# Optimization experiments

Measured on AMD Instinct MI355X. Metric: run time of the kernel, lower is better.

The kernel has to match this reference:

```python
import jax, jax.numpy as jnp
import numpy as np

V, D, H, DH, FF, L = 512, 256, 8, 32, 2048, 2
B, S = 4, 128
EPS = 1e-5


def setup_inputs() -> dict:
    key = jax.random.key(0)
    ks = jax.random.split(key, 8)
    rn = lambda k, shape: jax.random.normal(k, shape, jnp.float32) * 0.02
    return {
        "x_t": jax.random.randint(ks[0], (B, S), 0, V),
        "emb": rn(ks[1], (V, D)),
        "temperature": jnp.array(1.0, jnp.float32),
        "Wq": rn(ks[2], (L, D, D)), "Wk": rn(ks[3], (L, D, D)),
        "Wv": rn(ks[4], (L, D, D)), "Wo": rn(ks[5], (L, D, D)),
        "bq": jnp.zeros((L, D)), "bk": jnp.zeros((L, D)),
        "bv": jnp.zeros((L, D)), "bo": jnp.zeros((L, D)),
        "W1": rn(ks[6], (L, D, FF)), "b1": jnp.zeros((L, FF)),
        "W2": rn(ks[7], (L, FF, D)), "b2": jnp.zeros((L, D)),
        "ln1_s": jnp.ones((L, D)), "ln1_b": jnp.zeros((L, D)),
        "ln2_s": jnp.ones((L, D)), "ln2_b": jnp.zeros((L, D)),
    }


def _layer_norm(x, scale, bias):
    m = jnp.mean(x, axis=-1, keepdims=True)
    v = jnp.var(x, axis=-1, keepdims=True)
    return (x - m) / jnp.sqrt(v + EPS) * scale + bias


def reference(x_t, emb, temperature, Wq, Wk, Wv, Wo, bq, bk, bv, bo,
              W1, b1, W2, b2, ln1_s, ln1_b, ln2_s, ln2_b):
    b, s = x_t.shape
    x = emb[x_t]  # [B,S,D]
    scale = 1.0 / np.sqrt(DH).astype(np.float32)
    for l in range(L):  # 2 structurally distinct layers (post-norm, ReLU FFN)
        q = (x @ Wq[l] + bq[l]).reshape(b, s, H, DH)
        k = (x @ Wk[l] + bk[l]).reshape(b, s, H, DH)
        v = (x @ Wv[l] + bv[l]).reshape(b, s, H, DH)
        scores = jnp.einsum('bqhd,bkhd->bhqk', q, k) * scale
        attn = jax.nn.softmax(scores, axis=-1)
        o = jnp.einsum('bhqk,bkhd->bqhd', attn, v).reshape(b, s, D)
        x = _layer_norm(x + (o @ Wo[l] + bo[l]), ln1_s[l], ln1_b[l])
        ff = jax.nn.relu(x @ W1[l] + b1[l]) @ W2[l] + b2[l]
        x = _layer_norm(x + ff, ln2_s[l], ln2_b[l])
    sim = (x @ emb.T) / temperature            # [B,S,V]
    tp = jax.nn.softmax(sim, axis=-1)          # [B,S,V]
    # torch loop `trans_matrix[:,:,i,:] = transition_probs` == broadcast over row dim
    return jnp.broadcast_to(tp[:, :, None, :], (b, s, V, V))
```

## Files before the change

### kernel.cpp

```cpp
#include <hip/hip_runtime.h>
#include <math.h>

#define V_  512
#define D_  256
#define H_  8
#define DH_ 32
#define FF_ 2048
#define L_  2
#define B_  4
#define S_  128
#define T_  (B_*S_)

typedef float f32x4 __attribute__((ext_vector_type(4)));
typedef short s16x8 __attribute__((ext_vector_type(8)));
typedef unsigned short u16x4 __attribute__((ext_vector_type(4)));
typedef unsigned short ushort_t;

__device__ __forceinline__ ushort_t f2b(float f) {
    unsigned int u = __builtin_bit_cast(unsigned int, f);
    u += 0x7FFFu + ((u >> 16) & 1u);
    return (ushort_t)(u >> 16);
}
__device__ __forceinline__ float b2f(ushort_t h) {
    unsigned int u = ((unsigned int)h) << 16;
    return __builtin_bit_cast(float, u);
}

__device__ __forceinline__ float waveReduceSum(float v) {
#pragma unroll
    for (int off = 32; off > 0; off >>= 1) v += __shfl_xor(v, off);
    return v;
}
__device__ __forceinline__ float waveReduceMax(float v) {
#pragma unroll
    for (int off = 32; off > 0; off >>= 1) v = fmaxf(v, __shfl_xor(v, off));
    return v;
}

template<int RELU, int OUTB, int BIAS>
__device__ __forceinline__ void mgemm_body(
    const ushort_t* __restrict__ A, const ushort_t* __restrict__ BT,
    const float* __restrict__ bias, float* __restrict__ Cf,
    ushort_t* __restrict__ Cb, int M, int N, int K, int kBegin, int kSteps)
{
    __shared__ ushort_t Al[64][40];
    __shared__ ushort_t Bl[64][40];
    const int tid  = threadIdx.x;
    const int m0   = blockIdx.y * 64, n0 = blockIdx.x * 64;
    const int lane = tid & 63, w = tid >> 6;
    const int srow = tid >> 2, sseg = (tid & 3) * 8;
    const int l15  = lane & 15,  kg = (lane >> 4) * 8;

    f32x4 acc0 = {0.f,0.f,0.f,0.f}, acc1 = acc0, acc2 = acc0, acc3 = acc0;

    for (int kt = 0; kt < kSteps; ++kt) {
        const int k0 = kBegin + kt * 32;
        s16x8 av = *(const s16x8*)&A [(size_t)(m0 + srow) * K + k0 + sseg];
        s16x8 bv = *(const s16x8*)&BT[(size_t)(n0 + srow) * K + k0 + sseg];
        __syncthreads();
        *(s16x8*)&Al[srow][sseg] = av;
        *(s16x8*)&Bl[srow][sseg] = bv;
        __syncthreads();
        s16x8 bfr = *(const s16x8*)&Bl[w * 16 + l15][kg];
        s16x8 a0  = *(const s16x8*)&Al[     l15][kg];
        s16x8 a1  = *(const s16x8*)&Al[16 + l15][kg];
        s16x8 a2  = *(const s16x8*)&Al[32 + l15][kg];
        s16x8 a3  = *(const s16x8*)&Al[48 + l15][kg];
        acc0 = __builtin_amdgcn_mfma_f32_16x16x32_bf16(a0, bfr, acc0, 0, 0, 0);
        acc1 = __builtin_amdgcn_mfma_f32_16x16x32_bf16(a1, bfr, acc1, 0, 0, 0);
        acc2 = __builtin_amdgcn_mfma_f32_16x16x32_bf16(a2, bfr, acc2, 0, 0, 0);
        acc3 = __builtin_amdgcn_mfma_f32_16x16x32_bf16(a3, bfr, acc3, 0, 0, 0);
    }

    const int col = n0 + w * 16 + l15;
    const float bb = BIAS ? bias[col] : 0.f;
    f32x4 accs[4] = {acc0, acc1, acc2, acc3};
#pragma unroll
    for (int r = 0; r < 4; ++r) {
#pragma unroll
        for (int e = 0; e < 4; ++e) {
            const int row = m0 + r * 16 + (lane >> 4) * 4 + e;
            float v = accs[r][e] + bb;
            if (RELU) v = fmaxf(v, 0.f);
            if (OUTB) Cb[(size_t)row * N + col] = f2b(v);
            else      Cf[(size_t)row * N + col] = v;
        }
    }
}

template<int RELU, int OUTB, int BIAS>
__global__ __launch_bounds__(256) void mgemm_k(const ushort_t* A, const ushort_t* BT,
    const float* bias, float* Cf0, float* Cf1, ushort_t* Cb,
    int M, int N, int K, int kChunk)
{
    const int z = blockIdx.z;
    float* Cfz = nullptr;
    if (Cf0) Cfz = (z < 2) ? Cf0 + (size_t)z * M * N
                           : Cf1 + (size_t)(z - 2) * M * N;
    mgemm_body<RELU, OUTB, BIAS>(A, BT, bias, Cfz, Cb, M, N, K,
                                 z * kChunk, kChunk / 32);
}

__global__ __launch_bounds__(256) void qkv_k(const ushort_t* Xb, const ushort_t* WT,
    const float* bq, const float* bk, const float* bv,
    ushort_t* Qb, ushort_t* Kb, ushort_t* Vb)
{
    const int z = blockIdx.z;
    const ushort_t* bt = WT + (size_t)z * (D_ * D_);
    const float* bias; ushort_t* out;
    if (z == 0)      { bias = bq; out = Qb; }
    else if (z == 1) { bias = bk; out = Kb; }
    else             { bias = bv; out = Vb; }
    mgemm_body<0, 1, 1>(Xb, bt, bias, nullptr, out, T_, D_, D_, 0, D_ / 32);
}

__global__ __launch_bounds__(256) void prep_k(const int* __restrict__ xt,
    const float* __restrict__ emb, float* __restrict__ X,
    ushort_t* __restrict__ Xb, ushort_t* __restrict__ embB,
    const float* __restrict__ Wq, const float* __restrict__ Wk,
    const float* __restrict__ Wv, const float* __restrict__ Wo,
    const float* __restrict__ W1, const float* __restrict__ W2,
    ushort_t* __restrict__ WT, ushort_t* __restrict__ W1T, ushort_t* __restrict__ W2T)
{
    __shared__ float Tl[32][33];
    const int tid = threadIdx.x;
    if (blockIdx.x < 512) {
        const int idx = blockIdx.x * 256 + tid;
        const int t = idx >> 8, d = idx & 255;
        const float v = emb[(size_t)xt[t] * D_ + d];
        X[idx]  = v;
        Xb[idx] = f2b(v);
        embB[idx] = f2b(emb[idx]);
        return;
    }
    const int id = blockIdx.x - 512;
    const int l  = id >= 1280 ? 1 : 0;
    const int t  = id - l * 1280;
    const float* src; ushort_t* dst; int R, C, rt, ct;
    if (t < 256) {
        const int kind = t >> 6, tl = t & 63;
        const float* s0 = (kind == 0) ? Wq : (kind == 1) ? Wk : (kind == 2) ? Wv : Wo;
        src = s0 + (size_t)l * (D_ * D_);
        dst = WT + (size_t)l * (4 * D_ * D_) + (size_t)kind * (D_ * D_);
        R = D_; C = D_; rt = tl >> 3; ct = tl & 7;
    } else if (t < 768) {
        const int tl = t - 256;
        src = W1 + (size_t)l * (D_ * FF_); dst = W1T + (size_t)l * (D_ * FF_);
        R = D_; C = FF_; rt = tl >> 6; ct = tl & 63;
    } else {
        const int tl = t - 768;
        src = W2 + (size_t)l * (FF_ * D_); dst = W2T + (size_t)l * (FF_ * D_);
        R = FF_; C = D_; rt = tl >> 3; ct = tl & 7;
    }
    const int r = tid >> 3, c4 = (tid & 7) * 4;
    f32x4 v = *(const f32x4*)&src[(size_t)(rt * 32 + r) * C + ct * 32 + c4];
    Tl[r][c4] = v[0]; Tl[r][c4 + 1] = v[1]; Tl[r][c4 + 2] = v[2]; Tl[r][c4 + 3] = v[3];
    __syncthreads();
    u16x4 ov;
    ov[0] = f2b(Tl[c4 + 0][r]); ov[1] = f2b(Tl[c4 + 1][r]);
    ov[2] = f2b(Tl[c4 + 2][r]); ov[3] = f2b(Tl[c4 + 3][r]);
    *(u16x4*)&dst[(size_t)(ct * 32 + r) * R + rt * 32 + c4] = ov;
}

__global__ __launch_bounds__(256) void add_ln_k(
    const float* __restrict__ p0, const float* __restrict__ p1, int nparts,
    const float* __restrict__ bias, float* __restrict__ X,
    ushort_t* __restrict__ Xb, const float* __restrict__ s,
    const float* __restrict__ b)
{
    __shared__ float red[4];
    const int row = blockIdx.x, tid = threadIdx.x;
    const size_t off = (size_t)row * D_ + tid;
    const size_t TD = (size_t)T_ * D_;
    float a = X[off] + bias[tid] + p0[off];
    if (nparts == 4) a += p0[TD + off] + p1[off] + p1[TD + off];

    float ws_ = waveReduceSum(a);
    if ((tid & 63) == 0) red[tid >> 6] = ws_;
    __syncthreads();
    const float mean = (red[0] + red[1] + red[2] + red[3]) * (1.f / D_);
    __syncthreads();
    const float d = a - mean;
    float vs = waveReduceSum(d * d);
    if ((tid & 63) == 0) red[tid >> 6] = vs;
    __syncthreads();
    const float var = (red[0] + red[1] + red[2] + red[3]) * (1.f / D_);
    const float y = d * rsqrtf(var + 1e-5f) * s[tid] + b[tid];
    X[off]  = y;
    Xb[off] = f2b(y);
}

__global__ __launch_bounds__(256) void attn_k(const ushort_t* __restrict__ Qb,
    const ushort_t* __restrict__ Kb, const ushort_t* __restrict__ Vb,
    ushort_t* __restrict__ Ob)
{
    __shared__ float Qs[32][36], Ks[128][36], Vs[128][36], Ps[32][132];
    const int bh = blockIdx.x, b = bh >> 3, h = bh & 7;
    const int i0 = blockIdx.y * 32;
    const int tid = threadIdx.x;

#pragma unroll
    for (int it = 0; it < 2; ++it) {
        const int g = it * 256 + tid;
        const int r = g >> 2, c8 = (g & 3) * 8;
        s16x8 kv = *(const s16x8*)&Kb[(size_t)(b * S_ + r) * D_ + h * DH_ + c8];
        s16x8 vv = *(const s16x8*)&Vb[(size_t)(b * S_ + r) * D_ + h * DH_ + c8];
        f32x4 klo = {b2f((ushort_t)kv[0]), b2f((ushort_t)kv[1]), b2f((ushort_t)kv[2]), b2f((ushort_t)kv[3])};
        f32x4 khi = {b2f((ushort_t)kv[4]), b2f((ushort_t)kv[5]), b2f((ushort_t)kv[6]), b2f((ushort_t)kv[7])};
        f32x4 vlo = {b2f((ushort_t)vv[0]), b2f((ushort_t)vv[1]), b2f((ushort_t)vv[2]), b2f((ushort_t)vv[3])};
        f32x4 vhi = {b2f((ushort_t)vv[4]), b2f((ushort_t)vv[5]), b2f((ushort_t)vv[6]), b2f((ushort_t)vv[7])};
        *(f32x4*)&Ks[r][c8]     = klo;  *(f32x4*)&Ks[r][c8 + 4] = khi;
        *(f32x4*)&Vs[r][c8]     = vlo;  *(f32x4*)&Vs[r][c8 + 4] = vhi;
    }
    if (tid < 128) {
        const int r = tid >> 2, c8 = (tid & 3) * 8;
        s16x8 qv = *(const s16x8*)&Qb[(size_t)(b * S_ + i0 + r) * D_ + h * DH_ + c8];
        f32x4 qlo = {b2f((ushort_t)qv[0]), b2f((ushort_t)qv[1]), b2f((ushort_t)qv[2]), b2f((ushort_t)qv[3])};
        f32x4 qhi = {b2f((ushort_t)qv[4]), b2f((ushort_t)qv[5]), b2f((ushort_t)qv[6]), b2f((ushort_t)qv[7])};
        *(f32x4*)&Qs[r][c8] = qlo;  *(f32x4*)&Qs[r][c8 + 4] = qhi;
    }
    __syncthreads();

    const int i = tid >> 3, jg = tid & 7;
    const float sc = 0.17677669529663687f;
    float sv[16];
    float mx = -1e30f;
#pragma unroll
    for (int jj = 0; jj < 16; ++jj) {
        const int j = jg + jj * 8;
        f32x4 a4 = {0.f,0.f,0.f,0.f};
#pragma unroll
        for (int kk = 0; kk < 8; ++kk) {
            f32x4 q = *(const f32x4*)&Qs[i][kk * 4];
            f32x4 k = *(const f32x4*)&Ks[j][kk * 4];
            a4 += q * k;
        }
        const float sdot = (a4[0] + a4[1] + a4[2] + a4[3]) * sc;
        sv[jj] = sdot;
        mx = fmaxf(mx, sdot);
    }
    mx = fmaxf(mx, __shfl_xor(mx, 1));
    mx = fmaxf(mx, __shfl_xor(mx, 2));
    mx = fmaxf(mx, __shfl_xor(mx, 4));
    float sum = 0.f;
#pragma unroll
    for (int jj = 0; jj < 16; ++jj) {
        const float e = __expf(sv[jj] - mx);
        Ps[i][jg + jj * 8] = e;
        sum += e;
    }
    sum += __shfl_xor(sum, 1);
    sum += __shfl_xor(sum, 2);
    sum += __shfl_xor(sum, 4);
    const float inv = 1.f / sum;
    __syncthreads();

    const int dg = tid & 7;
    f32x4 o = {0.f,0.f,0.f,0.f};
#pragma unroll 4
    for (int j = 0; j < 128; ++j) {
        const float p = Ps[i][j];
        f32x4 vv = *(const f32x4*)&Vs[j][dg * 4];
        o += vv * p;
    }
    u16x4 ov;
    ov[0] = f2b(o[0] * inv); ov[1] = f2b(o[1] * inv);
    ov[2] = f2b(o[2] * inv); ov[3] = f2b(o[3] * inv);
    *(u16x4*)&Ob[(size_t)(b * S_ + i0 + i) * D_ + h * DH_ + dg * 4] = ov;
}

__global__ __launch_bounds__(256) void bcast_k(const float* __restrict__ Lg,
    const float* __restrict__ temp, float* __restrict__ out)
{
    __shared__ float row[V_];
    __shared__ float red[4];
    const int blk = blockIdx.x, t = blk >> 2, quarter = blk & 3;
    const int tid = threadIdx.x;
    const float rT = 1.f / temp[0];
    const float l0 = Lg[(size_t)t * V_ + tid] * rT;
    const float l1 = Lg[(size_t)t * V_ + 256 + tid] * rT;
    float m = waveReduceMax(fmaxf(l0, l1));
    if ((tid & 63) == 0) red[tid >> 6] = m;
    __syncthreads();
    m = fmaxf(fmaxf(red[0], red[1]), fmaxf(red[2], red[3]));
    __syncthreads();
    const float e0 = __expf(l0 - m), e1 = __expf(l1 - m);
    float sblk = waveReduceSum(e0 + e1);
    if ((tid & 63) == 0) red[tid >> 6] = sblk;
    __syncthreads();
    const float inv = 1.f / (red[0] + red[1] + red[2] + red[3]);
    row[tid] = e0 * inv;
    row[tid + 256] = e1 * inv;
    __syncthreads();

    const int c = tid & 127, ihalf = tid >> 7;
    f32x4 v = *(const f32x4*)&row[c * 4];
    f32x4* dst = (f32x4*)out + (size_t)t * V_ * (V_ / 4);
#pragma unroll 4
    for (int r = 0; r < 64; ++r) {
        const int i = quarter * 128 + ihalf + r * 2;
        __builtin_nontemporal_store(v, &dst[(size_t)i * (V_ / 4) + c]);
    }
}

extern "C" void kernel_launch(void* const* d_in, const int* in_sizes, int n_in,
                              void* d_out, int out_size, void* d_ws, size_t ws_size,
                              hipStream_t stream)
{
    const int*   x_t  = (const int*)  d_in[0];
    const float* emb  = (const float*)d_in[1];
    const float* temp = (const float*)d_in[2];
    const float* Wq   = (const float*)d_in[3];
    const float* Wk   = (const float*)d_in[4];
    const float* Wv   = (const float*)d_in[5];
    const float* Wo   = (const float*)d_in[6];
    const float* bq   = (const float*)d_in[7];
    const float* bk   = (const float*)d_in[8];
    const float* bv   = (const float*)d_in[9];
    const float* bo   = (const float*)d_in[10];
    const float* W1   = (const float*)d_in[11];
    const float* b1   = (const float*)d_in[12];
    const float* W2   = (const float*)d_in[13];
    const float* b2   = (const float*)d_in[14];
    const float* ln1s = (const float*)d_in[15];
    const float* ln1b = (const float*)d_in[16];
    const float* ln2s = (const float*)d_in[17];
    const float* ln2b = (const float*)d_in[18];

    float* out = (float*)d_out;
    char*  wsb = (char*)d_ws;

    float*    X     = (float*)   (wsb + 0);
    float*    PartA = (float*)   (wsb + 524288);
    float*    Lg    = PartA;
    ushort_t* Qb    = (ushort_t*)(wsb + 1572864);
    float*    PartB = (float*)   (wsb + 1572864);
    ushort_t* Kb    = (ushort_t*)(wsb + 1835008);
    ushort_t* Vb    = (ushort_t*)(wsb + 2097152);
    ushort_t* Ob    = (ushort_t*)(wsb + 2359296);
    ushort_t* Xb    = (ushort_t*)(wsb + 2621440);
    ushort_t* Ffb   = (ushort_t*)(wsb + 2883584);
    ushort_t* embB  = (ushort_t*)(wsb + 4980736);
    ushort_t* WT    = (ushort_t*)(wsb + 5242880);
    ushort_t* W1T   = (ushort_t*)(wsb + 6291456);
    ushort_t* W2T   = (ushort_t*)(wsb + 8388608);

    prep_k<<<3072, 256, 0, stream>>>(x_t, emb, X, Xb, embB,
                                     Wq, Wk, Wv, Wo, W1, W2, WT, W1T, W2T);

    for (int l = 0; l < L_; ++l) {
        const ushort_t* WTl  = WT  + (size_t)l * (4 * D_ * D_);
        const ushort_t* W1Tl = W1T + (size_t)l * (D_ * FF_);
        const ushort_t* W2Tl = W2T + (size_t)l * (FF_ * D_);

        qkv_k<<<dim3(4, 8, 3), 256, 0, stream>>>(
            Xb, WTl, bq + l * D_, bk + l * D_, bv + l * D_, Qb, Kb, Vb);

        attn_k<<<dim3(32, 4), 256, 0, stream>>>(Qb, Kb, Vb, Ob);

        mgemm_k<0, 0, 0><<<dim3(4, 8, 1), 256, 0, stream>>>(
            Ob, WTl + 3 * D_ * D_, nullptr, PartA, nullptr, nullptr,
            T_, D_, D_, D_);
        add_ln_k<<<T_, 256, 0, stream>>>(PartA, nullptr, 1, bo + l * D_,
                                         X, Xb, ln1s + l * D_, ln1b + l * D_);

        mgemm_k<1, 1, 1><<<dim3(32, 8, 1), 256, 0, stream>>>(
            Xb, W1Tl, b1 + l * FF_, nullptr, nullptr, Ffb, T_, FF_, D_, D_);

        mgemm_k<0, 0, 0><<<dim3(4, 8, 4), 256, 0, stream>>>(
            Ffb, W2Tl, nullptr, PartA, PartB, nullptr, T_, D_, FF_, FF_ / 4);
        add_ln_k<<<T_, 256, 0, stream>>>(PartA, PartB, 4, b2 + l * D_,
                                         X, Xb, ln2s + l * D_, ln2b + l * D_);
    }

    mgemm_k<0, 0, 0><<<dim3(8, 8, 1), 256, 0, stream>>>(
        Xb, embB, nullptr, Lg, nullptr, nullptr, T_, V_, D_, D_);

    bcast_k<<<T_ * 4, 256, 0, stream>>>(Lg, temp, out);
}
```

Baseline: 187.9 us.

## Double-buffer LDS tiles in MFMA GEMM to overlap global loads with compute

```diff
diff --git a/kernel.cpp b/kernel.cpp
--- a/kernel.cpp
+++ b/kernel.cpp
@@ -43,8 +43,8 @@
     const float* __restrict__ bias, float* __restrict__ Cf,
     ushort_t* __restrict__ Cb, int M, int N, int K, int kBegin, int kSteps)
 {
-    __shared__ ushort_t Al[64][40];
-    __shared__ ushort_t Bl[64][40];
+    __shared__ ushort_t Al[2][64][40];
+    __shared__ ushort_t Bl[2][64][40];
     const int tid  = threadIdx.x;
     const int m0   = blockIdx.y * 64, n0 = blockIdx.x * 64;
     const int lane = tid & 63, w = tid >> 6;
@@ -53,23 +53,37 @@
 
     f32x4 acc0 = {0.f,0.f,0.f,0.f}, acc1 = acc0, acc2 = acc0, acc3 = acc0;
 
+    const ushort_t* Aptr = &A [(size_t)(m0 + srow) * K + kBegin + sseg];
+    const ushort_t* Bptr = &BT[(size_t)(n0 + srow) * K + kBegin + sseg];
+
+    s16x8 av = *(const s16x8*)Aptr;
+    s16x8 bv = *(const s16x8*)Bptr;
+    *(s16x8*)&Al[0][srow][sseg] = av;
+    *(s16x8*)&Bl[0][srow][sseg] = bv;
+
     for (int kt = 0; kt < kSteps; ++kt) {
-        const int k0 = kBegin + kt * 32;
-        s16x8 av = *(const s16x8*)&A [(size_t)(m0 + srow) * K + k0 + sseg];
-        s16x8 bv = *(const s16x8*)&BT[(size_t)(n0 + srow) * K + k0 + sseg];
-        __syncthreads();
-        *(s16x8*)&Al[srow][sseg] = av;
-        *(s16x8*)&Bl[srow][sseg] = bv;
-        __syncthreads();
-        s16x8 bfr = *(const s16x8*)&Bl[w * 16 + l15][kg];
-        s16x8 a0  = *(const s16x8*)&Al[     l15][kg];
-        s16x8 a1  = *(const s16x8*)&Al[16 + l15][kg];
-        s16x8 a2  = *(const s16x8*)&Al[32 + l15][kg];
-        s16x8 a3  = *(const s16x8*)&Al[48 + l15][kg];
+        const int cur = kt & 1;
+        const bool more = (kt + 1 < kSteps);
+        if (more) {
+            av = *(const s16x8*)(Aptr + (size_t)(kt + 1) * 32);
+            bv = *(const s16x8*)(Bptr + (size_t)(kt + 1) * 32);
+        }
+        asm volatile("s_waitcnt lgkmcnt(0)\n\ts_barrier" ::: "memory");
+
+        s16x8 bfr = *(const s16x8*)&Bl[cur][w * 16 + l15][kg];
+        s16x8 a0  = *(const s16x8*)&Al[cur][     l15][kg];
+        s16x8 a1  = *(const s16x8*)&Al[cur][16 + l15][kg];
+        s16x8 a2  = *(const s16x8*)&Al[cur][32 + l15][kg];
+        s16x8 a3  = *(const s16x8*)&Al[cur][48 + l15][kg];
         acc0 = __builtin_amdgcn_mfma_f32_16x16x32_bf16(a0, bfr, acc0, 0, 0, 0);
         acc1 = __builtin_amdgcn_mfma_f32_16x16x32_bf16(a1, bfr, acc1, 0, 0, 0);
         acc2 = __builtin_amdgcn_mfma_f32_16x16x32_bf16(a2, bfr, acc2, 0, 0, 0);
         acc3 = __builtin_amdgcn_mfma_f32_16x16x32_bf16(a3, bfr, acc3, 0, 0, 0);
+
+        if (more) {
+            *(s16x8*)&Al[cur ^ 1][srow][sseg] = av;
+            *(s16x8*)&Bl[cur ^ 1][srow][sseg] = bv;
+        }
     }
 
     const int col = n0 + w * 16 + l15;
```

New measurement: 180.0 us. 4.2% less time.
